# Performance work log

Hardware: AMD Instinct MI355X
Metric: run time of the kernel (lower is better)

Reference implementation:

```python
import jax, jax.numpy as jnp
import numpy as np

B, S, H, NH = 1, 2048, 4096, 32
HD = H // NH
INV_NORM = 1.0 / np.sqrt(HD)


def _alibi_slopes(n_heads):
    # standard Bloom ALiBi slopes
    closest_pow2 = 2 ** int(np.floor(np.log2(n_heads)))
    base = 2.0 ** (-(2.0 ** -(np.log2(closest_pow2) - 3)))
    slopes = base ** np.arange(1, closest_pow2 + 1)
    if closest_pow2 != n_heads:
        extra_base = 2.0 ** (-(2.0 ** -(np.log2(2 * closest_pow2) - 3)))
        extra = extra_base ** np.arange(1, 2 * (n_heads - closest_pow2) + 1, 2)
        slopes = np.concatenate([slopes, extra])
    return slopes.astype(np.float32)


def setup_inputs() -> dict:
    key = jax.random.key(0)
    ks = jax.random.split(key, 6)
    hidden_states = jax.random.normal(ks[0], (B, S, H), dtype=jnp.float32)
    residual = jax.random.normal(ks[1], (B, S, H), dtype=jnp.float32)
    # ALiBi bias: slopes[h] * position, shape [B*NH, 1, S]
    slopes = jnp.asarray(_alibi_slopes(NH))  # [NH]
    pos = jnp.arange(S, dtype=jnp.float32)  # [S]
    alibi = (slopes[:, None] * pos[None, :])[:, None, :]  # [NH,1,S]
    alibi = jnp.tile(alibi, (B, 1, 1))  # [B*NH,1,S]
    # causal mask: True = masked out
    attention_mask = ~jnp.tril(jnp.ones((S, S), dtype=bool))[None, None]  # [1,1,S,S]
    qkv_w = jax.random.normal(ks[2], (3 * H, H), dtype=jnp.float32) * 0.02
    qkv_b = jax.random.normal(ks[3], (3 * H,), dtype=jnp.float32) * 0.02
    dense_w = jax.random.normal(ks[4], (H, H), dtype=jnp.float32) * 0.02
    dense_b = jax.random.normal(ks[5], (H,), dtype=jnp.float32) * 0.02
    return {
        "hidden_states": hidden_states,
        "residual": residual,
        "alibi": alibi,
        "attention_mask": attention_mask,
        "qkv_w": qkv_w,
        "qkv_b": qkv_b,
        "dense_w": dense_w,
        "dense_b": dense_b,
    }


def reference(hidden_states, residual, alibi, attention_mask, qkv_w, qkv_b, dense_w, dense_b):
    b, s, h = hidden_states.shape
    fused = hidden_states @ qkv_w.T + qkv_b  # [B,S,3H]
    fused = fused.reshape(b, s, NH, 3, HD)  # per-head interleaved q,k,v
    q, k, v = fused[..., 0, :], fused[..., 1, :], fused[..., 2, :]  # [B,S,NH,HD]
    # scores = beta*alibi + inv_norm * q @ k^T
    scores = jnp.einsum("bqnd,bknd->bnqk", q, k) * INV_NORM
    scores = scores + alibi.reshape(b, NH, 1, s)  # broadcast over q
    scores = jnp.where(attention_mask, jnp.finfo(scores.dtype).min, scores)
    probs = jax.nn.softmax(scores.astype(jnp.float32), axis=-1)  # [B,NH,S,S]
    ctx = jnp.einsum("bnqk,bknd->bqnd", probs, v).reshape(b, s, h)
    out = ctx @ dense_w.T + dense_b
    return residual + out  # dropout_add with p=0 / eval mode
```

## Files before the change

### kernel.cpp

```cpp
#include <hip/hip_runtime.h>
#include <cstdint>
#include <cstddef>

typedef unsigned short u16;
typedef __attribute__((ext_vector_type(8))) __bf16 bf16x8;
typedef __attribute__((ext_vector_type(4))) float f32x4;

#define S_LEN   2048
#define H_DIM   4096
#define NH_N    32
#define HD_N    128
#define QKV_LD  12288

__device__ __forceinline__ u16 f2b(float f) {
  union { float f; unsigned u; } v; v.f = f;
  unsigned r = v.u + 0x7fffu + ((v.u >> 16) & 1u);
  return (u16)(r >> 16);
}

__device__ __forceinline__ void gl2lds16(const void* g, void* l) {
  __builtin_amdgcn_global_load_lds((__attribute__((address_space(1))) void*)g,
                                   (__attribute__((address_space(3))) void*)l,
                                   16, 0, 0);
}

__global__ __launch_bounds__(256) void cvt_kernel(const float* __restrict__ src,
                                                  u16* __restrict__ dst, int n8) {
  int i = blockIdx.x * 256 + threadIdx.x;
  if (i >= n8) return;
  const float4* s4 = (const float4*)src;
  float4 a = s4[i * 2], b = s4[i * 2 + 1];
  union { u16 o[8]; uint4 v; } u;
  u.o[0] = f2b(a.x); u.o[1] = f2b(a.y); u.o[2] = f2b(a.z); u.o[3] = f2b(a.w);
  u.o[4] = f2b(b.x); u.o[5] = f2b(b.y); u.o[6] = f2b(b.z); u.o[7] = f2b(b.w);
  ((uint4*)dst)[i] = u.v;
}

template <int OUTF32>
__global__ __launch_bounds__(256, 2)
void gemm_kernel(const u16* __restrict__ A, const u16* __restrict__ B,
                 const float* __restrict__ bias, const float* __restrict__ resid,
                 u16* __restrict__ outB, float* __restrict__ outF,
                 int M, int N, int K) {
  __shared__ __align__(16) u16 As[128 * 64];
  __shared__ __align__(16) u16 Bs[128 * 64];
  const int tid  = threadIdx.x;
  const int lane = tid & 63;
  const int wave = tid >> 6;
  const int l15  = lane & 15;
  const int quad = lane >> 4;
  const int m0 = blockIdx.y * 128;
  const int n0 = blockIdx.x * 128;
  const int wm = (wave & 1) * 64;
  const int wn = (wave >> 1) * 64;

  f32x4 acc[4][4] = {};

  int sRow[4], sCol[4];
#pragma unroll
  for (int it = 0; it < 4; ++it) {
    int slot = wave * 256 + it * 64 + lane;
    int row  = slot >> 3;
    int kc   = (slot & 7) ^ (row & 7);
    sRow[it] = row;
    sCol[it] = kc * 8;
  }
  const u16* Ag = A + (size_t)m0 * K;
  const u16* Bg = B + (size_t)n0 * K;

  for (int kb = 0; kb < K; kb += 64) {
#pragma unroll
    for (int it = 0; it < 4; ++it) {
      int base = (wave * 256 + it * 64) * 8;
      gl2lds16(Ag + (size_t)sRow[it] * K + kb + sCol[it], &As[base]);
      gl2lds16(Bg + (size_t)sRow[it] * K + kb + sCol[it], &Bs[base]);
    }
    __syncthreads();
#pragma unroll
    for (int s = 0; s < 2; ++s) {
      const int kc = s * 4 + quad;
      bf16x8 af[4], bfr[4];
#pragma unroll
      for (int i = 0; i < 4; ++i) {
        int ra = wm + i * 16 + l15;
        af[i]  = *(const bf16x8*)&As[(ra * 8 + (kc ^ (ra & 7))) * 8];
        int rb = wn + i * 16 + l15;
        bfr[i] = *(const bf16x8*)&Bs[(rb * 8 + (kc ^ (rb & 7))) * 8];
      }
#pragma unroll
      for (int i = 0; i < 4; ++i)
#pragma unroll
        for (int j = 0; j < 4; ++j)
          acc[i][j] = __builtin_amdgcn_mfma_f32_16x16x32_bf16(af[i], bfr[j], acc[i][j], 0, 0, 0);
    }
    __syncthreads();
  }

  float bcol[4];
#pragma unroll
  for (int j = 0; j < 4; ++j) bcol[j] = bias[n0 + wn + j * 16 + l15];
#pragma unroll
  for (int i = 0; i < 4; ++i) {
    int rowb = m0 + wm + i * 16 + quad * 4;
#pragma unroll
    for (int r = 0; r < 4; ++r) {
      size_t rowoff = (size_t)(rowb + r) * N;
#pragma unroll
      for (int j = 0; j < 4; ++j) {
        int col = n0 + wn + j * 16 + l15;
        float v = acc[i][j][r] + bcol[j];
        if (OUTF32) outF[rowoff + col] = v + resid[rowoff + col];
        else        outB[rowoff + col] = f2b(v);
      }
    }
  }
}

__global__ __launch_bounds__(256, 2)
void attn_kernel(const u16* __restrict__ QKV, const float* __restrict__ alibi,
                 u16* __restrict__ CTX) {
  __shared__ __align__(16) u16 Ks[64 * 128];
  __shared__ __align__(16) u16 Vt[128 * 64];
  __shared__ __align__(16) u16 Ps[4 * 1024];
  const int tid  = threadIdx.x;
  const int lane = tid & 63;
  const int wave = tid >> 6;
  const int l15  = lane & 15;
  const int quad = lane >> 4;
  const int qt   = blockIdx.x;
  const int head = blockIdx.y;
  const int q0   = qt * 64;
  const int qcol = head * 384;
  const int kcol = qcol + 128;
  const int vcol = qcol + 256;
  const float c1 = 0.08838834764831845f * 1.4426950408889634f;
  const float slope2 = alibi[head * S_LEN + 1] * 1.4426950408889634f;

  bf16x8 qf[4];
  {
    const u16* qp = QKV + (size_t)(q0 + wave * 16 + l15) * QKV_LD + qcol;
#pragma unroll
    for (int s = 0; s < 4; ++s) qf[s] = *(const bf16x8*)(qp + s * 32 + quad * 8);
  }

  float m_i[4], l_i[4];
#pragma unroll
  for (int r = 0; r < 4; ++r) { m_i[r] = -3.0e38f; l_i[r] = 0.0f; }
  f32x4 acc[8] = {};

  const int nk = qt + 1;
  for (int kt = 0; kt < nk; ++kt) {
    const int k0 = kt * 64;
#pragma unroll
    for (int it = 0; it < 4; ++it) {
      int slot = wave * 256 + it * 64 + lane;
      int row  = slot >> 4;
      int hdc  = (slot & 15) ^ (row & 15);
      gl2lds16(QKV + (size_t)(k0 + row) * QKV_LD + kcol + hdc * 8,
               &Ks[(wave * 256 + it * 64) * 8]);
    }
#pragma unroll
    for (int it = 0; it < 4; ++it) {
      int c   = it * 256 + tid;
      int key = c & 63;
      int hd0 = (c >> 6) * 8;
      const u16* vp = QKV + (size_t)(k0 + key) * QKV_LD + vcol + hd0;
      union { uint4 v; u16 e[8]; } t; t.v = *(const uint4*)vp;
#pragma unroll
      for (int uu = 0; uu < 8; ++uu) {
        int hd = hd0 + uu;
        Vt[(hd * 8 + ((key >> 3) ^ (hd & 7))) * 8 + (key & 7)] = t.e[uu];
      }
    }
    __syncthreads();

    f32x4 sc[4] = {};
#pragma unroll
    for (int s = 0; s < 4; ++s) {
      const int kc = s * 4 + quad;
      bf16x8 kf[4];
#pragma unroll
      for (int j = 0; j < 4; ++j) {
        int row = j * 16 + l15;
        kf[j] = *(const bf16x8*)&Ks[(row * 16 + (kc ^ (row & 15))) * 8];
      }
#pragma unroll
      for (int j = 0; j < 4; ++j)
        sc[j] = __builtin_amdgcn_mfma_f32_16x16x32_bf16(qf[s], kf[j], sc[j], 0, 0, 0);
    }

    const bool diag = (kt == qt);
    float xv[4][4];
    float mt[4] = { -3.0e38f, -3.0e38f, -3.0e38f, -3.0e38f };
#pragma unroll
    for (int j = 0; j < 4; ++j) {
      int key  = k0 + j * 16 + l15;
      float al = slope2 * (float)key;
#pragma unroll
      for (int r = 0; r < 4; ++r) {
        float x = sc[j][r] * c1 + al;
        if (diag) {
          int qrow = q0 + wave * 16 + quad * 4 + r;
          if (key > qrow) x = -3.0e38f;
        }
        xv[j][r] = x;
        mt[r] = fmaxf(mt[r], x);
      }
    }
#pragma unroll
    for (int r = 0; r < 4; ++r) {
      float v = mt[r];
      v = fmaxf(v, __shfl_xor(v, 1));
      v = fmaxf(v, __shfl_xor(v, 2));
      v = fmaxf(v, __shfl_xor(v, 4));
      v = fmaxf(v, __shfl_xor(v, 8));
      mt[r] = fmaxf(m_i[r], v);
    }
    float alpha[4], psum[4];
#pragma unroll
    for (int r = 0; r < 4; ++r) {
      alpha[r] = exp2f(m_i[r] - mt[r]);
      m_i[r] = mt[r];
      psum[r] = 0.0f;
    }
#pragma unroll
    for (int j = 0; j < 4; ++j) {
      int col = j * 16 + l15;
      int kc  = col >> 3;
#pragma unroll
      for (int r = 0; r < 4; ++r) {
        float p = exp2f(xv[j][r] - m_i[r]);
        psum[r] += p;
        int qrow = quad * 4 + r;
        Ps[wave * 1024 + (qrow * 8 + (kc ^ (qrow & 7))) * 8 + (col & 7)] = f2b(p);
      }
    }
#pragma unroll
    for (int r = 0; r < 4; ++r) {
      float v = psum[r];
      v += __shfl_xor(v, 1);
      v += __shfl_xor(v, 2);
      v += __shfl_xor(v, 4);
      v += __shfl_xor(v, 8);
      l_i[r] = l_i[r] * alpha[r] + v;
    }
#pragma unroll
    for (int t = 0; t < 8; ++t)
#pragma unroll
      for (int r = 0; r < 4; ++r) acc[t][r] *= alpha[r];

#pragma unroll
    for (int s = 0; s < 2; ++s) {
      const int kc = s * 4 + quad;
      bf16x8 pf = *(const bf16x8*)&Ps[wave * 1024 + (l15 * 8 + (kc ^ (l15 & 7))) * 8];
#pragma unroll
      for (int t = 0; t < 8; ++t) {
        int row = t * 16 + l15;
        bf16x8 vf = *(const bf16x8*)&Vt[(row * 8 + (kc ^ (row & 7))) * 8];
        acc[t] = __builtin_amdgcn_mfma_f32_16x16x32_bf16(pf, vf, acc[t], 0, 0, 0);
      }
    }
    __syncthreads();
  }

#pragma unroll
  for (int r = 0; r < 4; ++r) {
    float inv = 1.0f / l_i[r];
    size_t rowoff = (size_t)(q0 + wave * 16 + quad * 4 + r) * H_DIM;
#pragma unroll
    for (int t = 0; t < 8; ++t)
      CTX[rowoff + head * HD_N + t * 16 + l15] = f2b(acc[t][r] * inv);
  }
}

extern "C" void kernel_launch(void* const* d_in, const int* in_sizes, int n_in,
                              void* d_out, int out_size, void* d_ws, size_t ws_size,
                              hipStream_t stream) {
  const float* hidden   = (const float*)d_in[0];
  const float* residual = (const float*)d_in[1];
  const float* alibi    = (const float*)d_in[2];
  const float* qkv_w    = (const float*)d_in[4];
  const float* qkv_b    = (const float*)d_in[5];
  const float* dense_w  = (const float*)d_in[6];
  const float* dense_b  = (const float*)d_in[7];
  float* out = (float*)d_out;

  u16* Xb  = (u16*)d_ws;
  u16* Wq  = Xb + (size_t)S_LEN * H_DIM;
  u16* Wd  = Wq + (size_t)3 * H_DIM * H_DIM;
  u16* QKV = Wd + (size_t)H_DIM * H_DIM;
  u16* CTX = QKV + (size_t)S_LEN * 3 * H_DIM;

  {
    int n8 = S_LEN * H_DIM / 8;
    cvt_kernel<<<dim3((n8 + 255) / 256), 256, 0, stream>>>(hidden, Xb, n8);
  }
  {
    int n8 = 3 * H_DIM * H_DIM / 8;
    cvt_kernel<<<dim3((n8 + 255) / 256), 256, 0, stream>>>(qkv_w, Wq, n8);
  }
  {
    int n8 = H_DIM * H_DIM / 8;
    cvt_kernel<<<dim3((n8 + 255) / 256), 256, 0, stream>>>(dense_w, Wd, n8);
  }

  gemm_kernel<0><<<dim3(3 * H_DIM / 128, S_LEN / 128), 256, 0, stream>>>(
      Xb, Wq, qkv_b, nullptr, QKV, nullptr, S_LEN, 3 * H_DIM, H_DIM);

  attn_kernel<<<dim3(S_LEN / 64, NH_N), 256, 0, stream>>>(QKV, alibi, CTX);

  gemm_kernel<1><<<dim3(H_DIM / 128, S_LEN / 128), 256, 0, stream>>>(
      CTX, Wd, dense_b, residual, nullptr, out, S_LEN, H_DIM, H_DIM);
}
```

Baseline: 862.2 us.

## Pair causal query tiles per block and double-buffer K/V staging in attention

Each attention block now handles two query tiles (bq and 31-bq), so every block does the same amount of causal work and the K/V tiles loaded for the long tile are reused by the short one. K and V shared tiles are double-buffered, with the next tile's loads issued before the current tile's compute, and V is transposed into LDS with packed 8-byte writes. The grid is halved to 512 blocks, and register and LDS use per block roughly double, which may limit occupancy.

```diff
diff --git a/kernel.cpp b/kernel.cpp
--- a/kernel.cpp
+++ b/kernel.cpp
@@ -119,62 +119,95 @@
 __global__ __launch_bounds__(256, 2)
 void attn_kernel(const u16* __restrict__ QKV, const float* __restrict__ alibi,
                  u16* __restrict__ CTX) {
-  __shared__ __align__(16) u16 Ks[64 * 128];
-  __shared__ __align__(16) u16 Vt[128 * 64];
-  __shared__ __align__(16) u16 Ps[4 * 1024];
+  __shared__ __align__(16) u16 Ks[2][64 * 128];
+  __shared__ __align__(16) u16 Vt[2][128 * 64];
+  __shared__ __align__(16) u16 Ps[8192];
   const int tid  = threadIdx.x;
   const int lane = tid & 63;
   const int wave = tid >> 6;
   const int l15  = lane & 15;
   const int quad = lane >> 4;
-  const int qt   = blockIdx.x;
+  const int bq   = blockIdx.x;
   const int head = blockIdx.y;
-  const int q0   = qt * 64;
+  const int gq0  = bq;
+  const int gq1  = 31 - bq;
+  const int nk   = 32 - bq;
   const int qcol = head * 384;
   const int kcol = qcol + 128;
   const int vcol = qcol + 256;
   const float c1 = 0.08838834764831845f * 1.4426950408889634f;
   const float slope2 = alibi[head * S_LEN + 1] * 1.4426950408889634f;
 
-  bf16x8 qf[4];
-  {
-    const u16* qp = QKV + (size_t)(q0 + wave * 16 + l15) * QKV_LD + qcol;
-#pragma unroll
-    for (int s = 0; s < 4; ++s) qf[s] = *(const bf16x8*)(qp + s * 32 + quad * 8);
-  }
-
-  float m_i[4], l_i[4];
-#pragma unroll
-  for (int r = 0; r < 4; ++r) { m_i[r] = -3.0e38f; l_i[r] = 0.0f; }
-  f32x4 acc[8] = {};
-
-  const int nk = qt + 1;
-  for (int kt = 0; kt < nk; ++kt) {
-    const int k0 = kt * 64;
+  const int keybase = (tid & 15) * 4;
+  const int hd0     = (tid >> 4) * 8;
+
+  auto stage_k = [&](int kt, int bb) {
 #pragma unroll
     for (int it = 0; it < 4; ++it) {
       int slot = wave * 256 + it * 64 + lane;
       int row  = slot >> 4;
       int hdc  = (slot & 15) ^ (row & 15);
-      gl2lds16(QKV + (size_t)(k0 + row) * QKV_LD + kcol + hdc * 8,
-               &Ks[(wave * 256 + it * 64) * 8]);
-    }
-#pragma unroll
-    for (int it = 0; it < 4; ++it) {
-      int c   = it * 256 + tid;
-      int key = c & 63;
-      int hd0 = (c >> 6) * 8;
-      const u16* vp = QKV + (size_t)(k0 + key) * QKV_LD + vcol + hd0;
-      union { uint4 v; u16 e[8]; } t; t.v = *(const uint4*)vp;
-#pragma unroll
-      for (int uu = 0; uu < 8; ++uu) {
-        int hd = hd0 + uu;
-        Vt[(hd * 8 + ((key >> 3) ^ (hd & 7))) * 8 + (key & 7)] = t.e[uu];
-      }
-    }
+      gl2lds16(QKV + (size_t)(kt * 64 + row) * QKV_LD + kcol + hdc * 8,
+               &Ks[bb][(wave * 256 + it * 64) * 8]);
+    }
+  };
+  auto load_v = [&](int kt, uint4* vr) {
+    const u16* vp = QKV + (size_t)(kt * 64 + keybase) * QKV_LD + vcol + hd0;
+#pragma unroll
+    for (int j = 0; j < 4; ++j) vr[j] = *(const uint4*)(vp + (size_t)j * QKV_LD);
+  };
+  auto write_v = [&](int bb, const uint4* vr) {
+    const u16* e0 = (const u16*)&vr[0];
+    const u16* e1 = (const u16*)&vr[1];
+    const u16* e2 = (const u16*)&vr[2];
+    const u16* e3 = (const u16*)&vr[3];
+#pragma unroll
+    for (int u = 0; u < 8; ++u) {
+      int hd = hd0 + u;
+      uint2 w;
+      w.x = (unsigned)e0[u] | ((unsigned)e1[u] << 16);
+      w.y = (unsigned)e2[u] | ((unsigned)e3[u] << 16);
+      *(uint2*)&Vt[bb][hd * 64 + ((keybase >> 3) ^ u) * 8 + (keybase & 7)] = w;
+    }
+  };
+
+  bf16x8 qf[2][4];
+#pragma unroll
+  for (int g = 0; g < 2; ++g) {
+    const int gqt = (g == 0) ? gq0 : gq1;
+    const u16* qp = QKV + (size_t)(gqt * 64 + wave * 16 + l15) * QKV_LD + qcol;
+#pragma unroll
+    for (int s = 0; s < 4; ++s) qf[g][s] = *(const bf16x8*)(qp + s * 32 + quad * 8);
+  }
+
+  float m_i[2][4], l_i[2][4];
+#pragma unroll
+  for (int g = 0; g < 2; ++g)
+#pragma unroll
+    for (int r = 0; r < 4; ++r) { m_i[g][r] = -3.0e38f; l_i[g][r] = 0.0f; }
+  f32x4 acc[2][8] = {};
+
+  {
+    stage_k(0, 0);
+    uint4 vr[4];
+    load_v(0, vr);
+    write_v(0, vr);
     __syncthreads();
-
-    f32x4 sc[4] = {};
+  }
+
+  for (int kt = 0; kt < nk; ++kt) {
+    const int cur = kt & 1;
+    const int nxt = cur ^ 1;
+    const bool more = (kt + 1 < nk);
+    uint4 vr[4];
+    if (more) { stage_k(kt + 1, nxt); load_v(kt + 1, vr); }
+
+    const int k0 = kt * 64;
+    const u16* Ksc = Ks[cur];
+    const u16* Vtc = Vt[cur];
+    const bool a0 = (kt <= gq0);
+
+    f32x4 sc[2][4] = {};
 #pragma unroll
     for (int s = 0; s < 4; ++s) {
       const int kc = s * 4 + quad;
@@ -182,94 +215,108 @@
 #pragma unroll
       for (int j = 0; j < 4; ++j) {
         int row = j * 16 + l15;
-        kf[j] = *(const bf16x8*)&Ks[(row * 16 + (kc ^ (row & 15))) * 8];
-      }
-#pragma unroll
-      for (int j = 0; j < 4; ++j)
-        sc[j] = __builtin_amdgcn_mfma_f32_16x16x32_bf16(qf[s], kf[j], sc[j], 0, 0, 0);
-    }
-
-    const bool diag = (kt == qt);
-    float xv[4][4];
-    float mt[4] = { -3.0e38f, -3.0e38f, -3.0e38f, -3.0e38f };
-#pragma unroll
-    for (int j = 0; j < 4; ++j) {
-      int key  = k0 + j * 16 + l15;
-      float al = slope2 * (float)key;
+        kf[j] = *(const bf16x8*)&Ksc[(row * 16 + (kc ^ (row & 15))) * 8];
+      }
+#pragma unroll
+      for (int j = 0; j < 4; ++j) {
+        sc[1][j] = __builtin_amdgcn_mfma_f32_16x16x32_bf16(qf[1][s], kf[j], sc[1][j], 0, 0, 0);
+        if (a0)
+          sc[0][j] = __builtin_amdgcn_mfma_f32_16x16x32_bf16(qf[0][s], kf[j], sc[0][j], 0, 0, 0);
+      }
+    }
+
+#pragma unroll
+    for (int g = 0; g < 2; ++g) {
+      if (g == 0 && !a0) continue;
+      const int gqt  = (g == 0) ? gq0 : gq1;
+      const bool diag = (kt == gqt);
+      const int qbase = gqt * 64 + wave * 16 + quad * 4;
+      float mt[4] = { -3.0e38f, -3.0e38f, -3.0e38f, -3.0e38f };
+#pragma unroll
+      for (int j = 0; j < 4; ++j) {
+        int key  = k0 + j * 16 + l15;
+        float al = slope2 * (float)key;
+#pragma unroll
+        for (int r = 0; r < 4; ++r) {
+          float x = sc[g][j][r] * c1 + al;
+          if (diag && key > qbase + r) x = -3.0e38f;
+          sc[g][j][r] = x;
+          mt[r] = fmaxf(mt[r], x);
+        }
+      }
 #pragma unroll
       for (int r = 0; r < 4; ++r) {
-        float x = sc[j][r] * c1 + al;
-        if (diag) {
-          int qrow = q0 + wave * 16 + quad * 4 + r;
-          if (key > qrow) x = -3.0e38f;
+        float v = mt[r];
+        v = fmaxf(v, __shfl_xor(v, 1));
+        v = fmaxf(v, __shfl_xor(v, 2));
+        v = fmaxf(v, __shfl_xor(v, 4));
+        v = fmaxf(v, __shfl_xor(v, 8));
+        mt[r] = fmaxf(m_i[g][r], v);
+      }
+      float psum[4];
+#pragma unroll
+      for (int r = 0; r < 4; ++r) {
+        float alpha = exp2f(m_i[g][r] - mt[r]);
+        m_i[g][r] = mt[r];
+        l_i[g][r] *= alpha;
+        psum[r] = 0.0f;
+#pragma unroll
+        for (int t = 0; t < 8; ++t) acc[g][t][r] *= alpha;
+      }
+#pragma unroll
+      for (int j = 0; j < 4; ++j) {
+        int col = j * 16 + l15;
+        int kc2 = col >> 3;
+#pragma unroll
+        for (int r = 0; r < 4; ++r) {
+          float p = exp2f(sc[g][j][r] - m_i[g][r]);
+          psum[r] += p;
+          int qrow = quad * 4 + r;
+          Ps[wave * 2048 + g * 1024 + (qrow * 8 + (kc2 ^ (qrow & 7))) * 8 + (col & 7)] = f2b(p);
         }
-        xv[j][r] = x;
-        mt[r] = fmaxf(mt[r], x);
-      }
-    }
-#pragma unroll
-    for (int r = 0; r < 4; ++r) {
-      float v = mt[r];
-      v = fmaxf(v, __shfl_xor(v, 1));
-      v = fmaxf(v, __shfl_xor(v, 2));
-      v = fmaxf(v, __shfl_xor(v, 4));
-      v = fmaxf(v, __shfl_xor(v, 8));
-      mt[r] = fmaxf(m_i[r], v);
-    }
-    float alpha[4], psum[4];
-#pragma unroll
-    for (int r = 0; r < 4; ++r) {
-      alpha[r] = exp2f(m_i[r] - mt[r]);
-      m_i[r] = mt[r];
-      psum[r] = 0.0f;
-    }
-#pragma unroll
-    for (int j = 0; j < 4; ++j) {
-      int col = j * 16 + l15;
-      int kc  = col >> 3;
+      }
 #pragma unroll
       for (int r = 0; r < 4; ++r) {
-        float p = exp2f(xv[j][r] - m_i[r]);
-        psum[r] += p;
-        int qrow = quad * 4 + r;
-        Ps[wave * 1024 + (qrow * 8 + (kc ^ (qrow & 7))) * 8 + (col & 7)] = f2b(p);
-      }
-    }
-#pragma unroll
-    for (int r = 0; r < 4; ++r) {
-      float v = psum[r];
-      v += __shfl_xor(v, 1);
-      v += __shfl_xor(v, 2);
-      v += __shfl_xor(v, 4);
-      v += __shfl_xor(v, 8);
-      l_i[r] = l_i[r] * alpha[r] + v;
-    }
-#pragma unroll
-    for (int t = 0; t < 8; ++t)
-#pragma unroll
-      for (int r = 0; r < 4; ++r) acc[t][r] *= alpha[r];
+        float v = psum[r];
+        v += __shfl_xor(v, 1);
+        v += __shfl_xor(v, 2);
+        v += __shfl_xor(v, 4);
+        v += __shfl_xor(v, 8);
+        l_i[g][r] += v;
+      }
+    }
 
 #pragma unroll
     for (int s = 0; s < 2; ++s) {
       const int kc = s * 4 + quad;
-      bf16x8 pf = *(const bf16x8*)&Ps[wave * 1024 + (l15 * 8 + (kc ^ (l15 & 7))) * 8];
+      bf16x8 pf1 = *(const bf16x8*)&Ps[wave * 2048 + 1024 + (l15 * 8 + (kc ^ (l15 & 7))) * 8];
+      bf16x8 pf0 = pf1;
+      if (a0) pf0 = *(const bf16x8*)&Ps[wave * 2048 + (l15 * 8 + (kc ^ (l15 & 7))) * 8];
 #pragma unroll
       for (int t = 0; t < 8; ++t) {
         int row = t * 16 + l15;
-        bf16x8 vf = *(const bf16x8*)&Vt[(row * 8 + (kc ^ (row & 7))) * 8];
-        acc[t] = __builtin_amdgcn_mfma_f32_16x16x32_bf16(pf, vf, acc[t], 0, 0, 0);
-      }
-    }
+        bf16x8 vf = *(const bf16x8*)&Vtc[(row * 8 + (kc ^ (row & 7))) * 8];
+        acc[1][t] = __builtin_amdgcn_mfma_f32_16x16x32_bf16(pf1, vf, acc[1][t], 0, 0, 0);
+        if (a0)
+          acc[0][t] = __builtin_amdgcn_mfma_f32_16x16x32_bf16(pf0, vf, acc[0][t], 0, 0, 0);
+      }
+    }
+
+    if (more) write_v(nxt, vr);
     __syncthreads();
   }
 
 #pragma unroll
-  for (int r = 0; r < 4; ++r) {
-    float inv = 1.0f / l_i[r];
-    size_t rowoff = (size_t)(q0 + wave * 16 + quad * 4 + r) * H_DIM;
-#pragma unroll
-    for (int t = 0; t < 8; ++t)
-      CTX[rowoff + head * HD_N + t * 16 + l15] = f2b(acc[t][r] * inv);
+  for (int g = 0; g < 2; ++g) {
+    const int gqt = (g == 0) ? gq0 : gq1;
+#pragma unroll
+    for (int r = 0; r < 4; ++r) {
+      float inv = 1.0f / l_i[g][r];
+      size_t rowoff = (size_t)(gqt * 64 + wave * 16 + quad * 4 + r) * H_DIM;
+#pragma unroll
+      for (int t = 0; t < 8; ++t)
+        CTX[rowoff + head * HD_N + t * 16 + l15] = f2b(acc[g][t][r] * inv);
+    }
   }
 }
 
@@ -307,7 +354,7 @@
   gemm_kernel<0><<<dim3(3 * H_DIM / 128, S_LEN / 128), 256, 0, stream>>>(
       Xb, Wq, qkv_b, nullptr, QKV, nullptr, S_LEN, 3 * H_DIM, H_DIM);
 
-  attn_kernel<<<dim3(S_LEN / 64, NH_N), 256, 0, stream>>>(QKV, alibi, CTX);
+  attn_kernel<<<dim3(16, NH_N), 256, 0, stream>>>(QKV, alibi, CTX);
 
   gemm_kernel<1><<<dim3(H_DIM / 128, S_LEN / 128), 256, 0, stream>>>(
       CTX, Wd, dense_b, residual, nullptr, out, S_LEN, H_DIM, H_DIM);
```

New measurement: 983.2 us. +14.0%, slower.

## Double-buffer K/V tiles via registers and balance causal attention block scheduling

Applied to the files above, without the earlier changes.

The attention kernel now prefetches the next K and V tiles into registers while computing the current tile, then writes them into a second LDS buffer after the PV MFMAs. This hides global-load latency behind compute. The grid is flattened to 1D with a permuted mapping from block index to (head, q-tile), so long and short causal tiles are interleaved across the device for better load balance. The V transpose now uses packed 64-bit LDS stores instead of scalar 16-bit stores. The cost is doubled LDS and extra registers, which may lower occupancy.

```diff
diff --git a/kernel.cpp b/kernel.cpp
--- a/kernel.cpp
+++ b/kernel.cpp
@@ -119,23 +119,68 @@
 __global__ __launch_bounds__(256, 2)
 void attn_kernel(const u16* __restrict__ QKV, const float* __restrict__ alibi,
                  u16* __restrict__ CTX) {
-  __shared__ __align__(16) u16 Ks[64 * 128];
-  __shared__ __align__(16) u16 Vt[128 * 64];
+  __shared__ __align__(16) u16 Ks[2][64 * 128];
+  __shared__ __align__(16) u16 Vt[2][128 * 64];
   __shared__ __align__(16) u16 Ps[4 * 1024];
   const int tid  = threadIdx.x;
   const int lane = tid & 63;
   const int wave = tid >> 6;
   const int l15  = lane & 15;
   const int quad = lane >> 4;
-  const int qt   = blockIdx.x;
-  const int head = blockIdx.y;
+
+  const int bidx = blockIdx.x;
+  const int t8   = bidx & 31;
+  const int h    = bidx >> 5;
+  const int head = h;
+  int A = (t8 + (h & 7)) & 31;
+  if (h & 16) A = (A + 8) & 31;
+  const int qt = (h & 8) ? (31 - A) : A;
+
   const int q0   = qt * 64;
+  const int nk   = qt + 1;
   const int qcol = head * 384;
   const int kcol = qcol + 128;
   const int vcol = qcol + 256;
   const float c1 = 0.08838834764831845f * 1.4426950408889634f;
   const float slope2 = alibi[head * S_LEN + 1] * 1.4426950408889634f;
 
+  const int krow = tid >> 2;
+  const int khd  = (tid & 3) * 32;
+  const int vkey = (tid & 15) * 4;
+  const int vhd  = (tid >> 4) * 8;
+
+  auto load_k = [&](int kt, uint4* kr) {
+    const uint4* p = (const uint4*)(QKV + (size_t)(kt * 64 + krow) * QKV_LD + kcol + khd);
+#pragma unroll
+    for (int c = 0; c < 4; ++c) kr[c] = p[c];
+  };
+  auto write_k = [&](int bb, const uint4* kr) {
+#pragma unroll
+    for (int c = 0; c < 4; ++c) {
+      int kc = (tid & 3) * 4 + c;
+      *(uint4*)&Ks[bb][(krow * 16 + (kc ^ (krow & 15))) * 8] = kr[c];
+    }
+  };
+  auto load_v = [&](int kt, uint4* vr) {
+    const u16* vp = QKV + (size_t)(kt * 64 + vkey) * QKV_LD + vcol + vhd;
+#pragma unroll
+    for (int j = 0; j < 4; ++j) vr[j] = *(const uint4*)(vp + (size_t)j * QKV_LD);
+  };
+  auto write_v = [&](int bb, const uint4* vr) {
+    const u16* e0 = (const u16*)&vr[0];
+    const u16* e1 = (const u16*)&vr[1];
+    const u16* e2 = (const u16*)&vr[2];
+    const u16* e3 = (const u16*)&vr[3];
+#pragma unroll
+    for (int u = 0; u < 8; ++u) {
+      int hd = vhd + u;
+      uint2 w;
+      w.x = (unsigned)e0[u] | ((unsigned)e1[u] << 16);
+      w.y = (unsigned)e2[u] | ((unsigned)e3[u] << 16);
+      *(uint2*)&Vt[bb][hd * 64 + ((vkey >> 3) ^ (hd & 7)) * 8 + (vkey & 7)] = w;
+    }
+  };
+
   bf16x8 qf[4];
   {
     const u16* qp = QKV + (size_t)(q0 + wave * 16 + l15) * QKV_LD + qcol;
@@ -148,31 +193,22 @@
   for (int r = 0; r < 4; ++r) { m_i[r] = -3.0e38f; l_i[r] = 0.0f; }
   f32x4 acc[8] = {};
 
-  const int nk = qt + 1;
+  {
+    uint4 kr[4], vr[4];
+    load_k(0, kr); load_v(0, vr);
+    write_k(0, kr); write_v(0, vr);
+    __syncthreads();
+  }
+
   for (int kt = 0; kt < nk; ++kt) {
+    const int cur = kt & 1;
+    const bool more = (kt + 1 < nk);
+    uint4 kr[4], vr[4];
+    if (more) { load_k(kt + 1, kr); load_v(kt + 1, vr); }
+
     const int k0 = kt * 64;
-#pragma unroll
-    for (int it = 0; it < 4; ++it) {
-      int slot = wave * 256 + it * 64 + lane;
-      int row  = slot >> 4;
-      int hdc  = (slot & 15) ^ (row & 15);
-      gl2lds16(QKV + (size_t)(k0 + row) * QKV_LD + kcol + hdc * 8,
-               &Ks[(wave * 256 + it * 64) * 8]);
-    }
-#pragma unroll
-    for (int it = 0; it < 4; ++it) {
-      int c   = it * 256 + tid;
-      int key = c & 63;
-      int hd0 = (c >> 6) * 8;
-      const u16* vp = QKV + (size_t)(k0 + key) * QKV_LD + vcol + hd0;
-      union { uint4 v; u16 e[8]; } t; t.v = *(const uint4*)vp;
-#pragma unroll
-      for (int uu = 0; uu < 8; ++uu) {
-        int hd = hd0 + uu;
-        Vt[(hd * 8 + ((key >> 3) ^ (hd & 7))) * 8 + (key & 7)] = t.e[uu];
-      }
-    }
-    __syncthreads();
+    const u16* Ksc = Ks[cur];
+    const u16* Vtc = Vt[cur];
 
     f32x4 sc[4] = {};
 #pragma unroll
@@ -182,7 +218,7 @@
 #pragma unroll
       for (int j = 0; j < 4; ++j) {
         int row = j * 16 + l15;
-        kf[j] = *(const bf16x8*)&Ks[(row * 16 + (kc ^ (row & 15))) * 8];
+        kf[j] = *(const bf16x8*)&Ksc[(row * 16 + (kc ^ (row & 15))) * 8];
       }
 #pragma unroll
       for (int j = 0; j < 4; ++j)
@@ -190,7 +226,6 @@
     }
 
     const bool diag = (kt == qt);
-    float xv[4][4];
     float mt[4] = { -3.0e38f, -3.0e38f, -3.0e38f, -3.0e38f };
 #pragma unroll
     for (int j = 0; j < 4; ++j) {
@@ -203,7 +238,7 @@
           int qrow = q0 + wave * 16 + quad * 4 + r;
           if (key > qrow) x = -3.0e38f;
         }
-        xv[j][r] = x;
+        sc[j][r] = x;
         mt[r] = fmaxf(mt[r], x);
       }
     }
@@ -216,23 +251,26 @@
       v = fmaxf(v, __shfl_xor(v, 8));
       mt[r] = fmaxf(m_i[r], v);
     }
-    float alpha[4], psum[4];
+    float psum[4];
 #pragma unroll
     for (int r = 0; r < 4; ++r) {
-      alpha[r] = exp2f(m_i[r] - mt[r]);
+      float alpha = exp2f(m_i[r] - mt[r]);
       m_i[r] = mt[r];
+      l_i[r] *= alpha;
       psum[r] = 0.0f;
+#pragma unroll
+      for (int u = 0; u < 8; ++u) acc[u][r] *= alpha;
     }
 #pragma unroll
     for (int j = 0; j < 4; ++j) {
       int col = j * 16 + l15;
-      int kc  = col >> 3;
+      int kc2 = col >> 3;
 #pragma unroll
       for (int r = 0; r < 4; ++r) {
-        float p = exp2f(xv[j][r] - m_i[r]);
+        float p = exp2f(sc[j][r] - m_i[r]);
         psum[r] += p;
         int qrow = quad * 4 + r;
-        Ps[wave * 1024 + (qrow * 8 + (kc ^ (qrow & 7))) * 8 + (col & 7)] = f2b(p);
+        Ps[wave * 1024 + (qrow * 8 + (kc2 ^ (qrow & 7))) * 8 + (col & 7)] = f2b(p);
       }
     }
 #pragma unroll
@@ -242,24 +280,22 @@
       v += __shfl_xor(v, 2);
       v += __shfl_xor(v, 4);
       v += __shfl_xor(v, 8);
-      l_i[r] = l_i[r] * alpha[r] + v;
-    }
-#pragma unroll
-    for (int t = 0; t < 8; ++t)
-#pragma unroll
-      for (int r = 0; r < 4; ++r) acc[t][r] *= alpha[r];
+      l_i[r] += v;
+    }
 
 #pragma unroll
     for (int s = 0; s < 2; ++s) {
       const int kc = s * 4 + quad;
       bf16x8 pf = *(const bf16x8*)&Ps[wave * 1024 + (l15 * 8 + (kc ^ (l15 & 7))) * 8];
 #pragma unroll
-      for (int t = 0; t < 8; ++t) {
-        int row = t * 16 + l15;
-        bf16x8 vf = *(const bf16x8*)&Vt[(row * 8 + (kc ^ (row & 7))) * 8];
-        acc[t] = __builtin_amdgcn_mfma_f32_16x16x32_bf16(pf, vf, acc[t], 0, 0, 0);
-      }
-    }
+      for (int u = 0; u < 8; ++u) {
+        int row = u * 16 + l15;
+        bf16x8 vf = *(const bf16x8*)&Vtc[(row * 8 + (kc ^ (row & 7))) * 8];
+        acc[u] = __builtin_amdgcn_mfma_f32_16x16x32_bf16(pf, vf, acc[u], 0, 0, 0);
+      }
+    }
+
+    if (more) { write_k(cur ^ 1, kr); write_v(cur ^ 1, vr); }
     __syncthreads();
   }
 
@@ -268,8 +304,8 @@
     float inv = 1.0f / l_i[r];
     size_t rowoff = (size_t)(q0 + wave * 16 + quad * 4 + r) * H_DIM;
 #pragma unroll
-    for (int t = 0; t < 8; ++t)
-      CTX[rowoff + head * HD_N + t * 16 + l15] = f2b(acc[t][r] * inv);
+    for (int u = 0; u < 8; ++u)
+      CTX[rowoff + head * HD_N + u * 16 + l15] = f2b(acc[u][r] * inv);
   }
 }
 
@@ -307,7 +343,7 @@
   gemm_kernel<0><<<dim3(3 * H_DIM / 128, S_LEN / 128), 256, 0, stream>>>(
       Xb, Wq, qkv_b, nullptr, QKV, nullptr, S_LEN, 3 * H_DIM, H_DIM);
 
-  attn_kernel<<<dim3(S_LEN / 64, NH_N), 256, 0, stream>>>(QKV, alibi, CTX);
+  attn_kernel<<<dim3(1024), 256, 0, stream>>>(QKV, alibi, CTX);
 
   gemm_kernel<1><<<dim3(H_DIM / 128, S_LEN / 128), 256, 0, stream>>>(
       CTX, Wd, dense_b, residual, nullptr, out, S_LEN, H_DIM, H_DIM);
```

Measured after the change: 870.9 us. About the same (+1.0%).
